# Kernel tuning notes

Measured on AMD Instinct MI355X. Metric: run time of the kernel, lower is better.

The kernel has to match this reference:

```python
import jax, jax.numpy as jnp
import numpy as np

N_NUM = 100        # numerical columns
N_CAT = 100        # categorical columns
CAT_COUNT = 100    # categories per categorical column
N_COND = 128
EPS = 1e-5         # torch GroupNorm default eps


def setup_inputs() -> dict:
    key = jax.random.key(0)
    ks = jax.random.split(key, 8)
    B = 4096
    return {
        "x_num": jax.random.normal(ks[0], (B, N_NUM), dtype=jnp.float32),
        "x_cat": jax.random.randint(ks[1], (B, N_CAT), 0, CAT_COUNT),
        "W_num": jax.random.normal(ks[2], (N_NUM, N_COND), dtype=jnp.float32),
        "b_num": jax.random.normal(ks[3], (N_NUM, N_COND), dtype=jnp.float32),
        "emb_table": jax.random.normal(ks[4], (N_CAT * CAT_COUNT, N_COND), dtype=jnp.float32),
        "gn_w": jnp.ones((N_CAT, N_COND), dtype=jnp.float32),
        "gn_b": jnp.zeros((N_CAT, N_COND), dtype=jnp.float32),
        "W_cat": jax.random.normal(ks[5], (N_CAT, N_COND, N_COND), dtype=jnp.float32) / np.sqrt(N_COND).astype(np.float32),
        "b_cat": jax.random.normal(ks[6], (N_CAT, N_COND), dtype=jnp.float32),
    }


def reference(x_num, x_cat, W_num, b_num, emb_table, gn_w, gn_b, W_cat, b_cat):
    # --- numerical branch: grouped 1x1 conv (Cin/g=1, Cout/g=n_cond) + sigmoid ---
    # (B, n_num, 1) * (n_num, n_cond) + bias -> (B, n_num, n_cond)
    num_emb = jax.nn.sigmoid(x_num[:, :, None] * W_num[None] + b_num[None])

    # --- categorical branch ---
    offsets = jnp.arange(N_CAT, dtype=x_cat.dtype) * CAT_COUNT  # cat_offset
    emb = emb_table[x_cat + offsets[None]]  # (B, n_cat, n_cond)

    # GroupNorm with n_cat groups over n_cat*n_cond channels (spatial dim = 1):
    # normalize each column's n_cond features per sample (biased variance).
    mean = jnp.mean(emb, axis=-1, keepdims=True)
    var = jnp.var(emb, axis=-1, keepdims=True)
    normed = (emb - mean) * jax.lax.rsqrt(var + EPS)
    normed = normed * gn_w[None] + gn_b[None]

    # grouped 1x1 conv, groups = n_cat: per-column n_cond x n_cond matmul
    cat_emb = jax.nn.sigmoid(jnp.einsum('bgi,gio->bgo', normed, W_cat) + b_cat[None])

    M = jnp.concatenate([num_emb, cat_emb], axis=1)  # (B, n_num+n_cat, n_cond)
    return jnp.transpose(M, (0, 2, 1))               # (B, n_cond, n_num+n_cat)
```

## Files before the change

kernel.cpp:

```cpp
#include <hip/hip_runtime.h>
#include <cstdint>

#define NNUM 100
#define NCAT 100
#define CATC 100
#define NCOND 128
#define GN_EPS 1e-5f

typedef __attribute__((ext_vector_type(8))) short bfrag8;
typedef __attribute__((ext_vector_type(4))) float accf4;

__device__ __forceinline__ float sigmoidf_(float x) { return 1.0f / (1.0f + __expf(-x)); }

__device__ __forceinline__ ushort f2bf(float f) {
    uint32_t u = __builtin_bit_cast(uint32_t, f);
    u += 0x7fffu + ((u >> 16) & 1u);
    return (ushort)(u >> 16);
}
__device__ __forceinline__ float bf2f(ushort h) {
    return __builtin_bit_cast(float, (uint32_t)h << 16);
}

__global__ __launch_bounds__(256)
void prep_wcat(const float* __restrict__ W_cat, ushort* __restrict__ Wf)
{
    const int g    = blockIdx.x;
    const int lane = threadIdx.x & 63;
    const int w    = threadIdx.x >> 6;
    const float* Wg = W_cat + ((size_t)g << 14);
    ushort* Wfg = Wf + ((size_t)g << 15);
    #pragma unroll
    for (int i = 0; i < 8; ++i) {
        int p  = w * 8 + i;
        int t  = p >> 2, kk = p & 3;
        int c  = t * 16 + (lane & 15);
        int kb = kk * 32 + ((lane >> 4) << 3);
        ushort hi[8], lo[8];
        #pragma unroll
        for (int j = 0; j < 8; ++j) {
            float v = Wg[(kb + j) * NCOND + c];
            ushort h = f2bf(v);
            hi[j] = h;
            lo[j] = f2bf(v - bf2f(h));
        }
        int off = ((t * 4 + kk) * 2) * 512 + lane * 8;
        *(bfrag8*)(Wfg + off)       = *(const bfrag8*)hi;
        *(bfrag8*)(Wfg + off + 512) = *(const bfrag8*)lo;
    }
}

template<int DIRECT>
__global__ __launch_bounds__(256, 2)
void cat_gemm_kernel(const int* __restrict__ x_cat,
                     const float* __restrict__ emb_table,
                     const float* __restrict__ gn_w,
                     const float* __restrict__ gn_b,
                     const ushort* __restrict__ Wf,
                     const float* __restrict__ b_cat,
                     float* __restrict__ dst)
{
    const int g    = blockIdx.y;
    const int b0   = blockIdx.x * 128;
    const int tid  = threadIdx.x;
    const int lane = tid & 63;
    const int w    = tid >> 6;

    __shared__ __align__(16) ushort Ahi[128 * 128];
    __shared__ __align__(16) ushort Alo[128 * 128];

    const int half = lane >> 5;
    const int l5   = lane & 31;
    float4 gwv = *(const float4*)(gn_w + g * NCOND + l5 * 4);
    float4 gbv = *(const float4*)(gn_b + g * NCOND + l5 * 4);

    int myidx = x_cat[(size_t)(b0 + w * 32 + (lane & 31)) * NCAT + g];

    #pragma unroll 8
    for (int it = 0; it < 16; ++it) {
        int r = it * 2 + half;
        int m = w * 32 + r;
        int idx = __shfl(myidx, r, 64);
        const float4* row = (const float4*)(emb_table + ((size_t)(g * CATC + idx) << 7));
        float4 v = row[l5];
        float s  = v.x + v.y + v.z + v.w;
        float ss = v.x * v.x + v.y * v.y + v.z * v.z + v.w * v.w;
        #pragma unroll
        for (int off = 16; off > 0; off >>= 1) {
            s  += __shfl_xor(s,  off, 64);
            ss += __shfl_xor(ss, off, 64);
        }
        float mean = s * 0.0078125f;
        float var  = fmaf(-mean, mean, ss * 0.0078125f);
        float rs   = rsqrtf(var + GN_EPS);
        float n0 = fmaf((v.x - mean) * rs, gwv.x, gbv.x);
        float n1 = fmaf((v.y - mean) * rs, gwv.y, gbv.y);
        float n2 = fmaf((v.z - mean) * rs, gwv.z, gbv.z);
        float n3 = fmaf((v.w - mean) * rs, gwv.w, gbv.w);
        ushort h0 = f2bf(n0), h1 = f2bf(n1), h2 = f2bf(n2), h3 = f2bf(n3);
        uint2 hp = { (uint32_t)h0 | ((uint32_t)h1 << 16),
                     (uint32_t)h2 | ((uint32_t)h3 << 16) };
        uint2 lp = { (uint32_t)f2bf(n0 - bf2f(h0)) | ((uint32_t)f2bf(n1 - bf2f(h1)) << 16),
                     (uint32_t)f2bf(n2 - bf2f(h2)) | ((uint32_t)f2bf(n3 - bf2f(h3)) << 16) };
        int bo = m * 256 + ((l5 * 8) ^ ((m & 7) << 4));
        *(uint2*)((char*)Ahi + bo) = hp;
        *(uint2*)((char*)Alo + bo) = lp;
    }
    asm volatile("s_waitcnt lgkmcnt(0)" ::: "memory");

    accf4 acc[2][8];
    #pragma unroll
    for (int gi = 0; gi < 2; ++gi)
        #pragma unroll
        for (int t = 0; t < 8; ++t)
            acc[gi][t] = (accf4){0.f, 0.f, 0.f, 0.f};

    const ushort* Wfg = Wf + ((size_t)g << 15);
    const int row0 = w * 32 + (lane & 15);
    const int sw   = (lane & 7) << 4;

    #pragma unroll
    for (int kk = 0; kk < 4; ++kk) {
        int colb = kk * 64 + ((lane >> 4) << 4);
        int o0 = row0 * 256 + (colb ^ sw);
        int o1 = o0 + 16 * 256;
        bfrag8 ah0 = *(const bfrag8*)((const char*)Ahi + o0);
        bfrag8 al0 = *(const bfrag8*)((const char*)Alo + o0);
        bfrag8 ah1 = *(const bfrag8*)((const char*)Ahi + o1);
        bfrag8 al1 = *(const bfrag8*)((const char*)Alo + o1);
        const ushort* wbase = Wfg + kk * 1024 + lane * 8;
        #pragma unroll
        for (int t = 0; t < 8; ++t) {
            bfrag8 wh = *(const bfrag8*)(wbase + t * 4096);
            bfrag8 wl = *(const bfrag8*)(wbase + t * 4096 + 512);
            acc[0][t] = __builtin_amdgcn_mfma_f32_16x16x32_bf16(ah0, wh, acc[0][t], 0, 0, 0);
            acc[0][t] = __builtin_amdgcn_mfma_f32_16x16x32_bf16(ah0, wl, acc[0][t], 0, 0, 0);
            acc[0][t] = __builtin_amdgcn_mfma_f32_16x16x32_bf16(al0, wh, acc[0][t], 0, 0, 0);
            acc[1][t] = __builtin_amdgcn_mfma_f32_16x16x32_bf16(ah1, wh, acc[1][t], 0, 0, 0);
            acc[1][t] = __builtin_amdgcn_mfma_f32_16x16x32_bf16(ah1, wl, acc[1][t], 0, 0, 0);
            acc[1][t] = __builtin_amdgcn_mfma_f32_16x16x32_bf16(al1, wh, acc[1][t], 0, 0, 0);
        }
    }

    const float* bcg = b_cat + g * NCOND;
    const int colL = lane & 15;
    const int quad = lane >> 4;
    #pragma unroll
    for (int t = 0; t < 8; ++t) {
        int c = t * 16 + colL;
        float bc = bcg[c];
        #pragma unroll
        for (int gi = 0; gi < 2; ++gi) {
            int mbase = (2 * w + gi) * 16 + quad * 4;
            #pragma unroll
            for (int r = 0; r < 4; ++r) {
                int b = b0 + mbase + r;
                float v = sigmoidf_(acc[gi][t][r] + bc);
                if (DIRECT) {
                    dst[(size_t)b * (128 * 200) + (size_t)c * 200 + 100 + g] = v;
                } else {
                    dst[(size_t)b * (NCAT * NCOND) + g * NCOND + c] = v;
                }
            }
        }
    }
}

__global__ __launch_bounds__(256)
void transpose_wn(const float* __restrict__ W_num, const float* __restrict__ b_num,
                  float* __restrict__ Wt, float* __restrict__ Bt)
{
    int idx = blockIdx.x * 256 + threadIdx.x;
    if (idx < NCOND * NNUM) {
        int c = idx / NNUM, j = idx - c * NNUM;
        Wt[idx] = W_num[j * NCOND + c];
        Bt[idx] = b_num[j * NCOND + c];
    }
}

__global__ __launch_bounds__(256)
void finalize_kernel(const float* __restrict__ ws_cat,
                     const float* __restrict__ Wt,
                     const float* __restrict__ Bt,
                     const float* __restrict__ x_num,
                     float* __restrict__ out)
{
    const int b   = blockIdx.x;
    const int h   = blockIdx.y;
    const int tid = threadIdx.x;
    __shared__ float T[NCAT * 65];
    __shared__ float xr[NNUM];

    if (tid < NNUM) xr[tid] = x_num[b * NNUM + tid];

    const float4* src = (const float4*)(ws_cat + (size_t)b * (NCAT * NCOND));
    #pragma unroll
    for (int it = 0; it < 7; ++it) {
        int i4 = it * 256 + tid;
        if (i4 < NCAT * 16) {
            int gg  = i4 >> 4;
            int cc4 = i4 & 15;
            float4 v = src[gg * 32 + h * 16 + cc4];
            float* d = &T[gg * 65 + cc4 * 4];
            d[0] = v.x; d[1] = v.y; d[2] = v.z; d[3] = v.w;
        }
    }
    __syncthreads();

    float4* outb = (float4*)(out + (size_t)b * (NCOND * 200)) + h * 3200;
    const float4* Wt4 = (const float4*)Wt;
    const float4* Bt4 = (const float4*)Bt;
    #pragma unroll
    for (int it = 0; it < 13; ++it) {
        int o4 = it * 256 + tid;
        if (o4 < 64 * 50) {
            int c_loc = o4 / 50;
            int j4    = o4 - c_loc * 50;
            int c     = h * 64 + c_loc;
            float4 v;
            if (j4 < 25) {
                float4 wv = Wt4[c * 25 + j4];
                float4 bv = Bt4[c * 25 + j4];
                int j = j4 * 4;
                v.x = sigmoidf_(fmaf(xr[j],     wv.x, bv.x));
                v.y = sigmoidf_(fmaf(xr[j + 1], wv.y, bv.y));
                v.z = sigmoidf_(fmaf(xr[j + 2], wv.z, bv.z));
                v.w = sigmoidf_(fmaf(xr[j + 3], wv.w, bv.w));
            } else {
                int gg = (j4 - 25) * 4;
                v.x = T[(gg    ) * 65 + c_loc];
                v.y = T[(gg + 1) * 65 + c_loc];
                v.z = T[(gg + 2) * 65 + c_loc];
                v.w = T[(gg + 3) * 65 + c_loc];
            }
            outb[o4] = v;
        }
    }
}

__global__ __launch_bounds__(256)
void num_direct(const float* __restrict__ x_num, const float* __restrict__ W_num,
                const float* __restrict__ b_num, float* __restrict__ out, int B)
{
    size_t i = (size_t)blockIdx.x * 256 + threadIdx.x;
    size_t total = (size_t)B * NCOND * NNUM;
    if (i >= total) return;
    int n = (int)(i % NNUM);
    size_t t = i / NNUM;
    int c = (int)(t % NCOND);
    int b = (int)(t / NCOND);
    float v = sigmoidf_(x_num[b * NNUM + n] * W_num[n * NCOND + c] + b_num[n * NCOND + c]);
    out[(size_t)b * (NCOND * 200) + (size_t)c * 200 + n] = v;
}

extern "C" void kernel_launch(void* const* d_in, const int* in_sizes, int n_in,
                              void* d_out, int out_size, void* d_ws, size_t ws_size,
                              hipStream_t stream)
{
    const float* x_num  = (const float*)d_in[0];
    const int*   x_cat  = (const int*)  d_in[1];
    const float* W_num  = (const float*)d_in[2];
    const float* b_num  = (const float*)d_in[3];
    const float* emb    = (const float*)d_in[4];
    const float* gn_w   = (const float*)d_in[5];
    const float* gn_b   = (const float*)d_in[6];
    const float* W_cat  = (const float*)d_in[7];
    const float* b_cat  = (const float*)d_in[8];
    float* out = (float*)d_out;

    const int B = in_sizes[0] / NNUM;
    const size_t cat_bytes = (size_t)B * NCAT * NCOND * sizeof(float);
    const size_t wtbt     = 2 * (size_t)NCOND * NNUM * sizeof(float);
    const size_t wf_bytes = (size_t)NCAT * 32768 * sizeof(ushort);
    const size_t need  = cat_bytes + wtbt;
    const size_t need2 = need + wf_bytes;

    dim3 gemm_grid(B / 128, NCAT);

    if (ws_size >= need) {
        float* ws_cat = (float*)d_ws;
        float* Wt = (float*)((char*)d_ws + cat_bytes);
        float* Bt = Wt + NCOND * NNUM;
        ushort* Wf = (ws_size >= need2) ? (ushort*)((char*)d_ws + need)
                                        : (ushort*)out;
        prep_wcat<<<NCAT, 256, 0, stream>>>(W_cat, Wf);
        transpose_wn<<<(NCOND * NNUM + 255) / 256, 256, 0, stream>>>(W_num, b_num, Wt, Bt);
        cat_gemm_kernel<0><<<gemm_grid, 256, 0, stream>>>(x_cat, emb, gn_w, gn_b, Wf, b_cat, ws_cat);
        finalize_kernel<<<dim3(B, 2), 256, 0, stream>>>(ws_cat, Wt, Bt, x_num, out);
    } else {
        ushort* Wf = (ushort*)d_ws;
        prep_wcat<<<NCAT, 256, 0, stream>>>(W_cat, Wf);
        cat_gemm_kernel<1><<<gemm_grid, 256, 0, stream>>>(x_cat, emb, gn_w, gn_b, Wf, b_cat, out);
        size_t total = (size_t)B * NCOND * NNUM;
        num_direct<<<(total + 255) / 256, 256, 0, stream>>>(x_num, W_num, b_num, out, B);
    }
}
```

Before: 624.7 us.

## Precompute per-category GEMM results and fold GroupNorm into affine epilogue

Since each embedding row comes from a fixed table of only 100 categories per column, the per-column matmul is applied once to the raw table rows (E = emb·diag(gn_w)·W) rather than once per batch sample. Row statistics (rstd, -mean·rstd) and the vectors Q = gn_w·W and P = gn_b·W + b_cat are precomputed, so each output becomes sigmoid(rs·E + nb·Q + P), gathered directly in the fused output kernel. This removes the batch-sized GEMM and the intermediate workspace round trip. In exchange it adds several small prep kernels, uses four split-bf16 MFMAs per product instead of three, and changes rounding because normalization is applied after the matmul.

```diff
diff --git a/kernel.cpp b/kernel.cpp
--- a/kernel.cpp
+++ b/kernel.cpp
@@ -22,12 +22,14 @@
 }
 
 __global__ __launch_bounds__(256)
-void prep_wcat(const float* __restrict__ W_cat, ushort* __restrict__ Wf)
+void prep_wcat(const float* __restrict__ W_cat, const float* __restrict__ gn_w,
+               ushort* __restrict__ Wf)
 {
     const int g    = blockIdx.x;
     const int lane = threadIdx.x & 63;
     const int w    = threadIdx.x >> 6;
     const float* Wg = W_cat + ((size_t)g << 14);
+    const float* gwg = gn_w + g * NCOND;
     ushort* Wfg = Wf + ((size_t)g << 15);
     #pragma unroll
     for (int i = 0; i < 8; ++i) {
@@ -38,7 +40,7 @@
         ushort hi[8], lo[8];
         #pragma unroll
         for (int j = 0; j < 8; ++j) {
-            float v = Wg[(kb + j) * NCOND + c];
+            float v = gwg[kb + j] * Wg[(kb + j) * NCOND + c];
             ushort h = f2bf(v);
             hi[j] = h;
             lo[j] = f2bf(v - bf2f(h));
@@ -49,18 +51,51 @@
     }
 }
 
-template<int DIRECT>
+__global__ __launch_bounds__(256)
+void prep_stats(const float* __restrict__ emb_table, float2* __restrict__ S)
+{
+    int r = blockIdx.x * 4 + (threadIdx.x >> 6);
+    int lane = threadIdx.x & 63;
+    if (r >= NCAT * CATC) return;
+    const float2* row = (const float2*)(emb_table + ((size_t)r << 7));
+    float2 v = row[lane];
+    float s  = v.x + v.y;
+    float ss = v.x * v.x + v.y * v.y;
+    #pragma unroll
+    for (int off = 32; off > 0; off >>= 1) {
+        s  += __shfl_xor(s,  off, 64);
+        ss += __shfl_xor(ss, off, 64);
+    }
+    float mean = s * 0.0078125f;
+    float var  = fmaf(-mean, mean, ss * 0.0078125f);
+    float rs   = rsqrtf(var + GN_EPS);
+    if (lane == 0) S[r] = make_float2(rs, -mean * rs);
+}
+
+__global__ __launch_bounds__(128)
+void prep_qp(const float* __restrict__ W_cat, const float* __restrict__ gn_w,
+             const float* __restrict__ gn_b, const float* __restrict__ b_cat,
+             float* __restrict__ Q, float* __restrict__ P)
+{
+    const int g = blockIdx.x, o = threadIdx.x;
+    const float* Wg = W_cat + ((size_t)g << 14);
+    float q = 0.f, p = 0.f;
+    #pragma unroll 4
+    for (int i = 0; i < NCOND; ++i) {
+        float wv = Wg[i * NCOND + o];
+        q = fmaf(gn_w[g * NCOND + i], wv, q);
+        p = fmaf(gn_b[g * NCOND + i], wv, p);
+    }
+    Q[g * NCOND + o] = q;
+    P[g * NCOND + o] = p + b_cat[g * NCOND + o];
+}
+
 __global__ __launch_bounds__(256, 2)
-void cat_gemm_kernel(const int* __restrict__ x_cat,
-                     const float* __restrict__ emb_table,
-                     const float* __restrict__ gn_w,
-                     const float* __restrict__ gn_b,
-                     const ushort* __restrict__ Wf,
-                     const float* __restrict__ b_cat,
-                     float* __restrict__ dst)
-{
-    const int g    = blockIdx.y;
-    const int b0   = blockIdx.x * 128;
+void prep_E_kernel(const float* __restrict__ emb_table,
+                   const ushort* __restrict__ Wf,
+                   float* __restrict__ E)
+{
+    const int g    = blockIdx.x;
     const int tid  = threadIdx.x;
     const int lane = tid & 63;
     const int w    = tid >> 6;
@@ -70,37 +105,19 @@
 
     const int half = lane >> 5;
     const int l5   = lane & 31;
-    float4 gwv = *(const float4*)(gn_w + g * NCOND + l5 * 4);
-    float4 gbv = *(const float4*)(gn_b + g * NCOND + l5 * 4);
-
-    int myidx = x_cat[(size_t)(b0 + w * 32 + (lane & 31)) * NCAT + g];
 
     #pragma unroll 8
     for (int it = 0; it < 16; ++it) {
         int r = it * 2 + half;
         int m = w * 32 + r;
-        int idx = __shfl(myidx, r, 64);
-        const float4* row = (const float4*)(emb_table + ((size_t)(g * CATC + idx) << 7));
+        int row_id = m < CATC ? m : (CATC - 1);
+        const float4* row = (const float4*)(emb_table + ((size_t)(g * CATC + row_id) << 7));
         float4 v = row[l5];
-        float s  = v.x + v.y + v.z + v.w;
-        float ss = v.x * v.x + v.y * v.y + v.z * v.z + v.w * v.w;
-        #pragma unroll
-        for (int off = 16; off > 0; off >>= 1) {
-            s  += __shfl_xor(s,  off, 64);
-            ss += __shfl_xor(ss, off, 64);
-        }
-        float mean = s * 0.0078125f;
-        float var  = fmaf(-mean, mean, ss * 0.0078125f);
-        float rs   = rsqrtf(var + GN_EPS);
-        float n0 = fmaf((v.x - mean) * rs, gwv.x, gbv.x);
-        float n1 = fmaf((v.y - mean) * rs, gwv.y, gbv.y);
-        float n2 = fmaf((v.z - mean) * rs, gwv.z, gbv.z);
-        float n3 = fmaf((v.w - mean) * rs, gwv.w, gbv.w);
-        ushort h0 = f2bf(n0), h1 = f2bf(n1), h2 = f2bf(n2), h3 = f2bf(n3);
+        ushort h0 = f2bf(v.x), h1 = f2bf(v.y), h2 = f2bf(v.z), h3 = f2bf(v.w);
         uint2 hp = { (uint32_t)h0 | ((uint32_t)h1 << 16),
                      (uint32_t)h2 | ((uint32_t)h3 << 16) };
-        uint2 lp = { (uint32_t)f2bf(n0 - bf2f(h0)) | ((uint32_t)f2bf(n1 - bf2f(h1)) << 16),
-                     (uint32_t)f2bf(n2 - bf2f(h2)) | ((uint32_t)f2bf(n3 - bf2f(h3)) << 16) };
+        uint2 lp = { (uint32_t)f2bf(v.x - bf2f(h0)) | ((uint32_t)f2bf(v.y - bf2f(h1)) << 16),
+                     (uint32_t)f2bf(v.z - bf2f(h2)) | ((uint32_t)f2bf(v.w - bf2f(h3)) << 16) };
         int bo = m * 256 + ((l5 * 8) ^ ((m & 7) << 4));
         *(uint2*)((char*)Ahi + bo) = hp;
         *(uint2*)((char*)Alo + bo) = lp;
@@ -135,31 +152,27 @@
             acc[0][t] = __builtin_amdgcn_mfma_f32_16x16x32_bf16(ah0, wh, acc[0][t], 0, 0, 0);
             acc[0][t] = __builtin_amdgcn_mfma_f32_16x16x32_bf16(ah0, wl, acc[0][t], 0, 0, 0);
             acc[0][t] = __builtin_amdgcn_mfma_f32_16x16x32_bf16(al0, wh, acc[0][t], 0, 0, 0);
+            acc[0][t] = __builtin_amdgcn_mfma_f32_16x16x32_bf16(al0, wl, acc[0][t], 0, 0, 0);
             acc[1][t] = __builtin_amdgcn_mfma_f32_16x16x32_bf16(ah1, wh, acc[1][t], 0, 0, 0);
             acc[1][t] = __builtin_amdgcn_mfma_f32_16x16x32_bf16(ah1, wl, acc[1][t], 0, 0, 0);
             acc[1][t] = __builtin_amdgcn_mfma_f32_16x16x32_bf16(al1, wh, acc[1][t], 0, 0, 0);
-        }
-    }
-
-    const float* bcg = b_cat + g * NCOND;
+            acc[1][t] = __builtin_amdgcn_mfma_f32_16x16x32_bf16(al1, wl, acc[1][t], 0, 0, 0);
+        }
+    }
+
+    float* Eg = E + (size_t)g * (CATC * NCOND);
     const int colL = lane & 15;
     const int quad = lane >> 4;
     #pragma unroll
     for (int t = 0; t < 8; ++t) {
         int c = t * 16 + colL;
-        float bc = bcg[c];
         #pragma unroll
         for (int gi = 0; gi < 2; ++gi) {
             int mbase = (2 * w + gi) * 16 + quad * 4;
             #pragma unroll
             for (int r = 0; r < 4; ++r) {
-                int b = b0 + mbase + r;
-                float v = sigmoidf_(acc[gi][t][r] + bc);
-                if (DIRECT) {
-                    dst[(size_t)b * (128 * 200) + (size_t)c * 200 + 100 + g] = v;
-                } else {
-                    dst[(size_t)b * (NCAT * NCOND) + g * NCOND + c] = v;
-                }
+                int m = mbase + r;
+                if (m < CATC) Eg[m * NCOND + c] = acc[gi][t][r];
             }
         }
     }
@@ -178,30 +191,53 @@
 }
 
 __global__ __launch_bounds__(256)
-void finalize_kernel(const float* __restrict__ ws_cat,
-                     const float* __restrict__ Wt,
-                     const float* __restrict__ Bt,
-                     const float* __restrict__ x_num,
-                     float* __restrict__ out)
+void fused_out_kernel(const int* __restrict__ x_cat,
+                      const float* __restrict__ x_num,
+                      const float* __restrict__ Wt,
+                      const float* __restrict__ Bt,
+                      const float* __restrict__ Q,
+                      const float* __restrict__ P,
+                      const float2* __restrict__ S,
+                      const float* __restrict__ E,
+                      float* __restrict__ out)
 {
     const int b   = blockIdx.x;
     const int h   = blockIdx.y;
     const int tid = threadIdx.x;
     __shared__ float T[NCAT * 65];
     __shared__ float xr[NNUM];
+    __shared__ float al[NCAT], be[NCAT];
+    __shared__ int   ei[NCAT];
 
     if (tid < NNUM) xr[tid] = x_num[b * NNUM + tid];
-
-    const float4* src = (const float4*)(ws_cat + (size_t)b * (NCAT * NCOND));
+    if (tid < NCAT) {
+        int idx = x_cat[(size_t)b * NCAT + tid];
+        ei[tid] = idx;
+        float2 s2 = S[tid * CATC + idx];
+        al[tid] = s2.x;
+        be[tid] = s2.y;
+    }
+    __syncthreads();
+
+    const float4* E4 = (const float4*)E;
+    const float4* Q4 = (const float4*)Q;
+    const float4* P4 = (const float4*)P;
     #pragma unroll
     for (int it = 0; it < 7; ++it) {
         int i4 = it * 256 + tid;
         if (i4 < NCAT * 16) {
-            int gg  = i4 >> 4;
-            int cc4 = i4 & 15;
-            float4 v = src[gg * 32 + h * 16 + cc4];
-            float* d = &T[gg * 65 + cc4 * 4];
-            d[0] = v.x; d[1] = v.y; d[2] = v.z; d[3] = v.w;
+            int g    = i4 >> 4;
+            int c4   = i4 & 15;
+            int col4 = h * 16 + c4;
+            float4 e = E4[(size_t)(g * CATC + ei[g]) * 32 + col4];
+            float4 q = Q4[g * 32 + col4];
+            float4 p = P4[g * 32 + col4];
+            float a = al[g], bb = be[g];
+            float* d = &T[g * 65 + c4 * 4];
+            d[0] = sigmoidf_(fmaf(a, e.x, fmaf(bb, q.x, p.x)));
+            d[1] = sigmoidf_(fmaf(a, e.y, fmaf(bb, q.y, p.y)));
+            d[2] = sigmoidf_(fmaf(a, e.z, fmaf(bb, q.z, p.z)));
+            d[3] = sigmoidf_(fmaf(a, e.w, fmaf(bb, q.w, p.w)));
         }
     }
     __syncthreads();
@@ -237,21 +273,6 @@
     }
 }
 
-__global__ __launch_bounds__(256)
-void num_direct(const float* __restrict__ x_num, const float* __restrict__ W_num,
-                const float* __restrict__ b_num, float* __restrict__ out, int B)
-{
-    size_t i = (size_t)blockIdx.x * 256 + threadIdx.x;
-    size_t total = (size_t)B * NCOND * NNUM;
-    if (i >= total) return;
-    int n = (int)(i % NNUM);
-    size_t t = i / NNUM;
-    int c = (int)(t % NCOND);
-    int b = (int)(t / NCOND);
-    float v = sigmoidf_(x_num[b * NNUM + n] * W_num[n * NCOND + c] + b_num[n * NCOND + c]);
-    out[(size_t)b * (NCOND * 200) + (size_t)c * 200 + n] = v;
-}
-
 extern "C" void kernel_launch(void* const* d_in, const int* in_sizes, int n_in,
                               void* d_out, int out_size, void* d_ws, size_t ws_size,
                               hipStream_t stream)
@@ -268,29 +289,19 @@
     float* out = (float*)d_out;
 
     const int B = in_sizes[0] / NNUM;
-    const size_t cat_bytes = (size_t)B * NCAT * NCOND * sizeof(float);
-    const size_t wtbt     = 2 * (size_t)NCOND * NNUM * sizeof(float);
-    const size_t wf_bytes = (size_t)NCAT * 32768 * sizeof(ushort);
-    const size_t need  = cat_bytes + wtbt;
-    const size_t need2 = need + wf_bytes;
-
-    dim3 gemm_grid(B / 128, NCAT);
-
-    if (ws_size >= need) {
-        float* ws_cat = (float*)d_ws;
-        float* Wt = (float*)((char*)d_ws + cat_bytes);
-        float* Bt = Wt + NCOND * NNUM;
-        ushort* Wf = (ws_size >= need2) ? (ushort*)((char*)d_ws + need)
-                                        : (ushort*)out;
-        prep_wcat<<<NCAT, 256, 0, stream>>>(W_cat, Wf);
-        transpose_wn<<<(NCOND * NNUM + 255) / 256, 256, 0, stream>>>(W_num, b_num, Wt, Bt);
-        cat_gemm_kernel<0><<<gemm_grid, 256, 0, stream>>>(x_cat, emb, gn_w, gn_b, Wf, b_cat, ws_cat);
-        finalize_kernel<<<dim3(B, 2), 256, 0, stream>>>(ws_cat, Wt, Bt, x_num, out);
-    } else {
-        ushort* Wf = (ushort*)d_ws;
-        prep_wcat<<<NCAT, 256, 0, stream>>>(W_cat, Wf);
-        cat_gemm_kernel<1><<<gemm_grid, 256, 0, stream>>>(x_cat, emb, gn_w, gn_b, Wf, b_cat, out);
-        size_t total = (size_t)B * NCOND * NNUM;
-        num_direct<<<(total + 255) / 256, 256, 0, stream>>>(x_num, W_num, b_num, out, B);
-    }
-}
+
+    float*  Wt = (float*)d_ws;
+    float*  Bt = Wt + NCOND * NNUM;
+    float*  Qb = Bt + NCOND * NNUM;
+    float*  Pb = Qb + NCAT * NCOND;
+    float2* Sb = (float2*)(Pb + NCAT * NCOND);
+    float*  Eb = (float*)(Sb + NCAT * CATC);
+    ushort* Wf = (ushort*)(Eb + NCAT * CATC * NCOND);
+
+    transpose_wn<<<(NCOND * NNUM + 255) / 256, 256, 0, stream>>>(W_num, b_num, Wt, Bt);
+    prep_wcat<<<NCAT, 256, 0, stream>>>(W_cat, gn_w, Wf);
+    prep_stats<<<(NCAT * CATC + 3) / 4, 256, 0, stream>>>(emb, Sb);
+    prep_qp<<<NCAT, 128, 0, stream>>>(W_cat, gn_w, gn_b, b_cat, Qb, Pb);
+    prep_E_kernel<<<NCAT, 256, 0, stream>>>(emb, Wf, Eb);
+    fused_out_kernel<<<dim3(B, 2), 256, 0, stream>>>(x_cat, x_num, Wt, Bt, Qb, Pb, Sb, Eb, out);
+}
```

New measurement: 513.4 us. 17.8% less time.
